# Kernel tuning notes

Hardware: AMD Instinct MI355X
Metric: run time of the kernel (lower is better)

## Reference

```python
import jax, jax.numpy as jnp
import numpy as np

D_MODEL = 256
N_LAYERS = 4
D_STATE = 16
D_CONV = 4
EXPAND = 2
HEADDIM = 64
D_INNER = EXPAND * D_MODEL            # 512
NHEADS = D_INNER // HEADDIM           # 8
CONV_DIM = D_INNER + 2 * D_STATE      # 544 (ngroups=1)
D_IN_PROJ = 2 * D_INNER + 2 * D_STATE + NHEADS  # 1064
VOCAB = 8
MAXLEN = 2048
NCLASSES = 2
PAD_IDX = 4
EPS = 1e-5
B, L = 8, 2048


def setup_inputs() -> dict:
    key = jax.random.key(0)
    ks = jax.random.split(key, 10)
    x = jax.random.randint(ks[0], (B, L), 0, VOCAB)
    attention_mask = jnp.ones((B, L), jnp.float32)
    embedding = 0.02 * jax.random.normal(ks[1], (VOCAB, D_MODEL), jnp.float32)
    embedding = embedding.at[PAD_IDX].set(0.0)  # padding_idx row is zero
    pos_embedding = 0.02 * jax.random.normal(ks[2], (1, MAXLEN, D_MODEL), jnp.float32)
    in_proj_w = 0.05 * jax.random.normal(ks[3], (N_LAYERS, D_IN_PROJ, D_MODEL), jnp.float32)
    conv_w = 0.3 * jax.random.normal(ks[4], (N_LAYERS, CONV_DIM, D_CONV), jnp.float32)
    conv_b = jnp.zeros((N_LAYERS, CONV_DIM), jnp.float32)
    # dt_bias = softplus^{-1}(dt) with dt ~ U(0.001, 0.1), as in mamba_ssm init
    dt = jax.random.uniform(ks[5], (N_LAYERS, NHEADS), jnp.float32, 0.001, 0.1)
    dt_bias = jnp.log(jnp.expm1(dt))
    A_log = jnp.log(jax.random.uniform(ks[6], (N_LAYERS, NHEADS), jnp.float32, 1.0, 16.0))
    D_param = jnp.ones((N_LAYERS, NHEADS), jnp.float32)
    norm_w = jnp.ones((N_LAYERS, D_INNER), jnp.float32)
    out_proj_w = 0.05 * jax.random.normal(ks[7], (N_LAYERS, D_MODEL, D_INNER), jnp.float32)
    ln_w = jnp.ones((D_MODEL,), jnp.float32)
    ln_b = jnp.zeros((D_MODEL,), jnp.float32)
    cls_w = 0.05 * jax.random.normal(ks[8], (NCLASSES, D_MODEL), jnp.float32)
    cls_b = jnp.zeros((NCLASSES,), jnp.float32)
    return dict(x=x, attention_mask=attention_mask, embedding=embedding,
                pos_embedding=pos_embedding, in_proj_w=in_proj_w, conv_w=conv_w,
                conv_b=conv_b, dt_bias=dt_bias, A_log=A_log, D_param=D_param,
                norm_w=norm_w, out_proj_w=out_proj_w, ln_w=ln_w, ln_b=ln_b,
                cls_w=cls_w, cls_b=cls_b)


def _mamba2(h_in, Wi, cw, cb, dtb, Alog, Dp, nw, Wo):
    """One Mamba2 block (ngroups=1, headdim=64, norm_before_gate=False)."""
    b, l, _ = h_in.shape
    zxbcdt = jnp.einsum('bld,ed->ble', h_in, Wi)          # (b,l,1064)
    z = zxbcdt[..., :D_INNER]                             # gate
    xBC = zxbcdt[..., D_INNER:D_INNER + CONV_DIM]
    dt = jax.nn.softplus(zxbcdt[..., D_INNER + CONV_DIM:] + dtb)  # (b,l,h)
    # causal depthwise conv1d (kernel D_CONV) + silu
    xp = jnp.pad(xBC, ((0, 0), (D_CONV - 1, 0), (0, 0)))
    xwin = jnp.stack([xp[:, k:k + l, :] for k in range(D_CONV)], axis=-1)  # (b,l,c,k)
    xBC = jax.nn.silu(jnp.einsum('blck,ck->blc', xwin, cw) + cb)
    xs = xBC[..., :D_INNER].reshape(b, l, NHEADS, HEADDIM)
    Bm = xBC[..., D_INNER:D_INNER + D_STATE]              # (b,l,n)
    Cm = xBC[..., D_INNER + D_STATE:]                     # (b,l,n)
    dA = jnp.exp(dt * (-jnp.exp(Alog)))                   # (b,l,h)
    dtx = dt[..., None] * xs                              # (b,l,h,p)

    def step(h, inp):
        dA_t, dtx_t, B_t, C_t = inp
        h = dA_t[:, :, None, None] * h + dtx_t[..., None] * B_t[:, None, None, :]
        y = jnp.einsum('bhpn,bn->bhp', h, C_t)
        return h, y

    h0 = jnp.zeros((b, NHEADS, HEADDIM, D_STATE), h_in.dtype)
    _, ys = jax.lax.scan(step, h0, (jnp.swapaxes(dA, 0, 1), jnp.swapaxes(dtx, 0, 1),
                                    jnp.swapaxes(Bm, 0, 1), jnp.swapaxes(Cm, 0, 1)))
    y = jnp.swapaxes(ys, 0, 1) + Dp[None, None, :, None] * xs  # skip term D*x
    y = y.reshape(b, l, D_INNER) * jax.nn.silu(z)               # gate, then RMSNorm
    y = y * jax.lax.rsqrt(jnp.mean(jnp.square(y), axis=-1, keepdims=True) + EPS) * nw
    return jnp.einsum('ble,de->bld', y, Wo)


def _layer_norm(h, w, b):
    mu = jnp.mean(h, -1, keepdims=True)
    var = jnp.mean(jnp.square(h - mu), -1, keepdims=True)
    return (h - mu) * jax.lax.rsqrt(var + EPS) * w + b


def reference(x, attention_mask, embedding, pos_embedding, in_proj_w, conv_w,
              conv_b, dt_bias, A_log, D_param, norm_w, out_proj_w, ln_w, ln_b,
              cls_w, cls_b):
    l = x.shape[1]
    h = embedding[x] + pos_embedding[:, :l, :]
    m = attention_mask[..., None]
    h = h * m
    for i in range(N_LAYERS):
        res = h
        h = _mamba2(h, in_proj_w[i], conv_w[i], conv_b[i], dt_bias[i],
                    A_log[i], D_param[i], norm_w[i], out_proj_w[i])
        h = _layer_norm(h + res, ln_w, ln_b)
        h = h * m
    pooled = jnp.mean(h, axis=1)   # dropout is identity at eval
    return pooled @ cls_w.T + cls_b
```

## Files before the change

kernel.cpp:

```cpp
#include <hip/hip_runtime.h>
#include <hip/hip_bf16.h>
#include <math.h>

#define B_ 8
#define L_ 2048
#define DM 256
#define DIP 1064
#define DI 512
#define CD 544
#define DSZ 16
#define NH 8
#define HD 64
#define Q_ 64
#define NC 32
#define ZST 76

typedef __attribute__((ext_vector_type(8))) short bf16x8;
typedef __attribute__((ext_vector_type(4))) float f32x4;

__device__ inline unsigned short f2bf(float f) {
    __hip_bfloat16 h = __float2bfloat16(f);
    return *(unsigned short*)&h;
}
__device__ inline float bf2f(unsigned short u) {
    unsigned int x = ((unsigned int)u) << 16;
    return __uint_as_float(x);
}
__device__ inline float fast_sig(float x) {
    return __builtin_amdgcn_rcpf(1.f + __expf(-x));
}

__global__ __launch_bounds__(256) void k_f2bf(const float* __restrict__ in, unsigned short* __restrict__ out, int n4) {
    int i = blockIdx.x * 256 + threadIdx.x;
    if (i >= n4) return;
    float4 v = *(const float4*)(in + (size_t)i * 4);
    ushort4 o;
    o.x = f2bf(v.x); o.y = f2bf(v.y); o.z = f2bf(v.z); o.w = f2bf(v.w);
    *(ushort4*)(out + (size_t)i * 4) = o;
}

__global__ __launch_bounds__(256) void k_embed(const int* __restrict__ x, const float* __restrict__ mask,
                                               const float* __restrict__ emb, const float* __restrict__ pos,
                                               unsigned short* __restrict__ h_bf) {
    int i = blockIdx.x * 256 + threadIdx.x;
    if (i >= B_ * L_ * DM) return;
    int d = i % DM;
    int bl = i / DM;
    int l = bl % L_;
    int tok = x[bl];
    float v = (emb[tok * DM + d] + pos[l * DM + d]) * mask[bl];
    h_bf[i] = f2bf(v);
}

__global__ __launch_bounds__(256) void k_gemm_in(const unsigned short* __restrict__ A,
                                                 const unsigned short* __restrict__ Bw,
                                                 unsigned short* __restrict__ Cb, float* __restrict__ dtraw) {
    const int lda = DM, ldb = DM, ldc = DIP, N = DIP, K = DM;
    __shared__ unsigned short Al[2][128 * 32];
    __shared__ unsigned short Bl[2][128 * 32];
    int tid = threadIdx.x;
    int l = tid & 63;
    int w = tid >> 6, wr = w >> 1, wc = w & 1;

    int wg = blockIdx.x;
    int xcd = wg & 7;
    int rest = wg >> 3;
    int mgrp = rest / 9;
    int n_tile = rest - mgrp * 9;
    int m_tile = xcd * 16 + mgrp;
    int m0 = m_tile * 128, n0 = n_tile * 128;

    f32x4 zero = {0.f, 0.f, 0.f, 0.f};
    f32x4 acc[4][4];
#pragma unroll
    for (int i = 0; i < 4; i++)
#pragma unroll
        for (int j = 0; j < 4; j++) acc[i][j] = zero;

    int lr = l & 15, kq = l >> 4;
    int aoff = (wr * 64 + lr) * 32 + kq * 8;
    int boff = (wc * 64 + lr) * 32 + kq * 8;

    auto stage = [&](int ks, int buf) {
        int k0 = ks * 32;
#pragma unroll
        for (int q = 0; q < 2; q++) {
            int c = tid + q * 256;
            int row = c >> 2, cc = (c & 3) * 8;
            const unsigned short* ga = A + (size_t)(m0 + row) * lda + k0 + cc;
            __builtin_amdgcn_global_load_lds((const __attribute__((address_space(1))) void*)ga,
                                             (__attribute__((address_space(3))) void*)(&Al[buf][c * 8]), 16, 0, 0);
            int rowb = n0 + row;
            if (rowb > N - 1) rowb = N - 1;
            const unsigned short* gb = Bw + (size_t)rowb * ldb + k0 + cc;
            __builtin_amdgcn_global_load_lds((const __attribute__((address_space(1))) void*)gb,
                                             (__attribute__((address_space(3))) void*)(&Bl[buf][c * 8]), 16, 0, 0);
        }
    };

    stage(0, 0);
    int ksteps = K / 32;
    for (int s = 0; s < ksteps; s++) {
        int buf = s & 1;
        __syncthreads();
        if (s + 1 < ksteps) stage(s + 1, buf ^ 1);
        bf16x8 a[4], b[4];
#pragma unroll
        for (int i = 0; i < 4; i++) a[i] = *(const bf16x8*)&Al[buf][aoff + i * 512];
#pragma unroll
        for (int j = 0; j < 4; j++) b[j] = *(const bf16x8*)&Bl[buf][boff + j * 512];
#pragma unroll
        for (int i = 0; i < 4; i++)
#pragma unroll
            for (int j = 0; j < 4; j++)
                acc[i][j] = __builtin_amdgcn_mfma_f32_16x16x32_bf16(a[i], b[j], acc[i][j], 0, 0, 0);
    }

#pragma unroll
    for (int i = 0; i < 4; i++) {
        int m = m0 + wr * 64 + i * 16 + kq * 4;
#pragma unroll
        for (int j = 0; j < 4; j++) {
            int n = n0 + wc * 64 + j * 16 + lr;
            if (n < N) {
#pragma unroll
                for (int r = 0; r < 4; r++)
                    Cb[(size_t)(m + r) * ldc + n] = f2bf(acc[i][j][r]);
                if (n >= DI + CD) {
#pragma unroll
                    for (int r = 0; r < 4; r++)
                        dtraw[(size_t)(m + r) * NH + (n - (DI + CD))] = acc[i][j][r];
                }
            }
        }
    }
}

__global__ __launch_bounds__(256) void k_gemm_ln(const unsigned short* __restrict__ A,
                                                 const unsigned short* __restrict__ Bw,
                                                 unsigned short* __restrict__ hbf,
                                                 const float* __restrict__ lnw, const float* __restrict__ lnb,
                                                 const float* __restrict__ mask) {
    __shared__ unsigned short Al[2][32 * 32];
    __shared__ unsigned short Bl[2][256 * 32];
    __shared__ float part_s[32][4], part_q[32][4];
    int tid = threadIdx.x;
    int l = tid & 63;
    int w = tid >> 6;
    int m0 = blockIdx.x * 32;
    int lr = l & 15, kq = l >> 4;

    f32x4 zero = {0.f, 0.f, 0.f, 0.f};
    f32x4 acc[2][4];
#pragma unroll
    for (int i = 0; i < 2; i++)
#pragma unroll
        for (int j = 0; j < 4; j++) acc[i][j] = zero;

    auto stage = [&](int ks, int buf) {
        int k0 = ks * 32;
        if (tid < 128) {
            int row = tid >> 2, cc = (tid & 3) * 8;
            const unsigned short* ga = A + (size_t)(m0 + row) * DI + k0 + cc;
            __builtin_amdgcn_global_load_lds((const __attribute__((address_space(1))) void*)ga,
                                             (__attribute__((address_space(3))) void*)(&Al[buf][tid * 8]), 16, 0, 0);
        }
#pragma unroll
        for (int q = 0; q < 4; q++) {
            int c = tid + q * 256;
            int row = c >> 2, cc = (c & 3) * 8;
            const unsigned short* gb = Bw + (size_t)row * DI + k0 + cc;
            __builtin_amdgcn_global_load_lds((const __attribute__((address_space(1))) void*)gb,
                                             (__attribute__((address_space(3))) void*)(&Bl[buf][c * 8]), 16, 0, 0);
        }
    };

    stage(0, 0);
    const int ksteps = DI / 32;
    for (int s = 0; s < ksteps; s++) {
        int buf = s & 1;
        __syncthreads();
        if (s + 1 < ksteps) stage(s + 1, buf ^ 1);
        bf16x8 a[2], b[4];
#pragma unroll
        for (int i = 0; i < 2; i++) a[i] = *(const bf16x8*)&Al[buf][(i * 16 + lr) * 32 + kq * 8];
#pragma unroll
        for (int j = 0; j < 4; j++) b[j] = *(const bf16x8*)&Bl[buf][(w * 64 + j * 16 + lr) * 32 + kq * 8];
#pragma unroll
        for (int i = 0; i < 2; i++)
#pragma unroll
            for (int j = 0; j < 4; j++)
                acc[i][j] = __builtin_amdgcn_mfma_f32_16x16x32_bf16(a[i], b[j], acc[i][j], 0, 0, 0);
    }

#pragma unroll
    for (int i = 0; i < 2; i++) {
#pragma unroll
        for (int r = 0; r < 4; r++) {
            int row = i * 16 + kq * 4 + r;
            const unsigned short* hrow = hbf + (size_t)(m0 + row) * DM + w * 64 + lr;
#pragma unroll
            for (int j = 0; j < 4; j++)
                acc[i][j][r] += bf2f(hrow[j * 16]);
        }
    }
#pragma unroll
    for (int i = 0; i < 2; i++) {
#pragma unroll
        for (int r = 0; r < 4; r++) {
            float sv = acc[i][0][r] + acc[i][1][r] + acc[i][2][r] + acc[i][3][r];
            float qv = acc[i][0][r] * acc[i][0][r] + acc[i][1][r] * acc[i][1][r] +
                       acc[i][2][r] * acc[i][2][r] + acc[i][3][r] * acc[i][3][r];
#pragma unroll
            for (int off = 1; off < 16; off <<= 1) {
                sv += __shfl_xor(sv, off);
                qv += __shfl_xor(qv, off);
            }
            if (lr == 0) {
                int row = i * 16 + kq * 4 + r;
                part_s[row][w] = sv;
                part_q[row][w] = qv;
            }
        }
    }
    __syncthreads();
    float4 wv4 = make_float4(lnw[w * 64 + 0 * 16 + lr], lnw[w * 64 + 1 * 16 + lr],
                             lnw[w * 64 + 2 * 16 + lr], lnw[w * 64 + 3 * 16 + lr]);
    float4 bv4 = make_float4(lnb[w * 64 + 0 * 16 + lr], lnb[w * 64 + 1 * 16 + lr],
                             lnb[w * 64 + 2 * 16 + lr], lnb[w * 64 + 3 * 16 + lr]);
#pragma unroll
    for (int i = 0; i < 2; i++) {
#pragma unroll
        for (int r = 0; r < 4; r++) {
            int row = i * 16 + kq * 4 + r;
            float sum = part_s[row][0] + part_s[row][1] + part_s[row][2] + part_s[row][3];
            float sq  = part_q[row][0] + part_q[row][1] + part_q[row][2] + part_q[row][3];
            float mu = sum * (1.f / DM);
            float var = sq * (1.f / DM) - mu * mu;
            float rs = rsqrtf(var + 1e-5f);
            float mk = mask[m0 + row];
            unsigned short* drow = hbf + (size_t)(m0 + row) * DM + w * 64 + lr;
            float wr_[4] = {wv4.x, wv4.y, wv4.z, wv4.w};
            float br_[4] = {bv4.x, bv4.y, bv4.z, bv4.w};
#pragma unroll
            for (int j = 0; j < 4; j++) {
                float o = ((acc[i][j][r] - mu) * rs * wr_[j] + br_[j]) * mk;
                drow[j * 16] = f2bf(o);
            }
        }
    }
}

__global__ __launch_bounds__(256) void k_bcdt(const unsigned short* __restrict__ zxb,
                                              const float* __restrict__ cw, const float* __restrict__ cb,
                                              const float* __restrict__ dtraw, const float* __restrict__ dtb,
                                              const float* __restrict__ Alog,
                                              unsigned short* __restrict__ BCc,
                                              float* __restrict__ dts_g, float* __restrict__ coefS_g,
                                              float* __restrict__ cumL, float* __restrict__ Pg) {
    int pair = blockIdx.x;
    int b = pair >> 5, c = pair & 31;
    int t0 = c * Q_;
    int tid = threadIdx.x;
    int t = tid & 63, oct = tid >> 6;
    {
        int lg0 = t0 + t - 3;
        const unsigned short* base = zxb + ((size_t)b * L_ + lg0) * DIP + 1024 + oct * 8;
        bf16x8 rows[4];
#pragma unroll
        for (int k = 0; k < 4; k++) {
            if (lg0 + k >= 0) rows[k] = *(const bf16x8*)(base + (size_t)k * DIP);
            else {
#pragma unroll
                for (int j = 0; j < 8; j++) rows[k][j] = 0;
            }
        }
        bf16x8 o;
#pragma unroll
        for (int j = 0; j < 8; j++) {
            int cc = DI + oct * 8 + j;
            float acc = cb[cc];
            acc = fmaf(bf2f((unsigned short)rows[0][j]), cw[cc * 4 + 0], acc);
            acc = fmaf(bf2f((unsigned short)rows[1][j]), cw[cc * 4 + 1], acc);
            acc = fmaf(bf2f((unsigned short)rows[2][j]), cw[cc * 4 + 2], acc);
            acc = fmaf(bf2f((unsigned short)rows[3][j]), cw[cc * 4 + 3], acc);
            float s = acc * fast_sig(acc);
            o[j] = (short)f2bf(s);
        }
        *(bf16x8*)(BCc + ((size_t)(b * L_ + t0 + t)) * 32 + oct * 8) = o;
    }
#pragma unroll
    for (int ho = 0; ho < 2; ho++) {
        int h = oct * 2 + ho;
        int bh = b * 8 + h;
        float raw = dtraw[(size_t)(b * L_ + t0 + t) * NH + h] + dtb[h];
        float dtv = (raw > 20.f) ? raw : log1pf(__expf(raw));
        float v = -__expf(Alog[h]) * dtv;
#pragma unroll
        for (int off = 1; off < 64; off <<= 1) {
            float u = __shfl_up(v, off);
            if (t >= off) v += u;
        }
        float lend = __shfl(v, 63);
        size_t base = (size_t)(bh * NC + c) * Q_ + t;
        dts_g[base] = dtv;
        cumL[base] = v;
        coefS_g[base] = __expf(lend - v) * dtv;
        if (t == 63) Pg[bh * NC + c] = __expf(v);
    }
}

__global__ __launch_bounds__(256) void k_scan1c(const unsigned short* __restrict__ zxb,
                                                const unsigned short* __restrict__ BCc,
                                                const float* __restrict__ dts_g, const float* __restrict__ coefS_g,
                                                const float* __restrict__ cumL,
                                                const float* __restrict__ cw, const float* __restrict__ cb,
                                                const float* __restrict__ Dp,
                                                unsigned short* __restrict__ ybuf, unsigned short* __restrict__ Sg) {
    int wg = blockIdx.x;
    int xcd = wg & 7;
    int rest = wg >> 3;
    int slot = rest >> 3;
    int h = rest & 7;
    int pair = slot * 8 + xcd;
    int b = pair >> 5, c = pair & 31;
    int bh = b * 8 + h;
    int tid = threadIdx.x;
    int t0 = c * Q_;
    int w = tid >> 6, l = tid & 63;
    int lr = l & 15, kq = l >> 4;

    __shared__ __align__(16) unsigned short Zl[67 * ZST];
    __shared__ __align__(16) unsigned short Xt[Q_ * 72];
    __shared__ __align__(16) unsigned short Cbf[Q_ * 32];
    __shared__ __align__(16) unsigned short Bbf[Q_ * 32];
    __shared__ __align__(16) unsigned short Btw[DSZ * 72];
    __shared__ float Lc[Q_], dts[Q_], coefS[Q_];
    unsigned short* Mbf = Zl;

    float Dval = Dp[h];

    for (int idx = tid; idx < 67 * 8; idx += 256) {
        int rr = idx >> 3, seg = idx & 7;
        int lg = t0 - 3 + rr;
        bf16x8 v;
        if (lg >= 0) {
            v = *(const bf16x8*)(zxb + (size_t)(b * L_ + lg) * DIP + DI + h * HD + seg * 8);
        } else {
#pragma unroll
            for (int j = 0; j < 8; j++) v[j] = 0;
        }
        *(ushort4*)&Zl[rr * ZST + seg * 8]     = *(ushort4*)&v;
        *(ushort4*)&Zl[rr * ZST + seg * 8 + 4] = *((ushort4*)&v + 1);
    }
    {
        bf16x8 z8;
#pragma unroll
        for (int j = 0; j < 8; j++) z8[j] = 0;
        *(bf16x8*)&Cbf[tid * 8] = z8;
        *(bf16x8*)&Bbf[tid * 8] = z8;
    }
    if (tid < 64) {
        size_t base = (size_t)(bh * NC + c) * Q_ + tid;
        dts[tid] = dts_g[base];
        Lc[tid] = cumL[base];
        coefS[tid] = coefS_g[base];
    }
    __syncthreads();

    float xreg[4][4];
#pragma unroll
    for (int pt = 0; pt < 4; pt++) {
#pragma unroll
        for (int r = 0; r < 4; r++) {
            int t = w * 16 + kq * 4 + r;
            int p = pt * 16 + lr;
            int cc = h * HD + p;
            float acc = cb[cc];
#pragma unroll
            for (int k = 0; k < 4; k++)
                acc = fmaf(bf2f(Zl[(t + k) * ZST + p]), cw[cc * 4 + k], acc);
            float s = acc * fast_sig(acc);
            xreg[pt][r] = s;
            Xt[p * 72 + t] = f2bf(s);
        }
    }
    {
        int t = tid & 63, oct = tid >> 6;
        bf16x8 v = *(const bf16x8*)(BCc + ((size_t)(b * L_ + t0 + t)) * 32 + oct * 8);
        float dtv = dts[t], cfv = coefS[t];
#pragma unroll
        for (int j = 0; j < 8; j++) {
            int n32 = oct * 8 + j;
            float s = bf2f((unsigned short)v[j]);
            if (n32 < 16) {
                int n = n32;
                Bbf[t * 32 + (((n >> 3) ^ (t & 3)) * 8) + (n & 7)] = f2bf(dtv * s);
                Btw[n * 72 + t] = f2bf(cfv * s);
            } else {
                int n = n32 - 16;
                Cbf[t * 32 + (((n >> 3) ^ (t & 3)) * 8) + (n & 7)] = (unsigned short)v[j];
            }
        }
    }
    __syncthreads();

    f32x4 zero = {0.f, 0.f, 0.f, 0.f};

    f32x4 cbt[4];
    {
        bf16x8 af = *(const bf16x8*)&Cbf[(w * 16 + lr) * 32 + ((kq ^ (lr & 3)) * 8)];
#pragma unroll
        for (int st = 0; st < 4; st++) {
            bf16x8 bf = *(const bf16x8*)&Bbf[(st * 16 + lr) * 32 + ((kq ^ (lr & 3)) * 8)];
            cbt[st] = __builtin_amdgcn_mfma_f32_16x16x32_bf16(af, bf, zero, 0, 0, 0);
        }
    }
#pragma unroll
    for (int st = 0; st < 4; st++) {
#pragma unroll
        for (int r = 0; r < 4; r++) {
            int t = w * 16 + kq * 4 + r;
            int s = st * 16 + lr;
            float m = (s <= t) ? __expf(Lc[t] - Lc[s]) * cbt[st][r] : 0.f;
            Mbf[t * 64 + (((s >> 3) ^ (t & 7)) * 8) + (s & 7)] = f2bf(m);
        }
    }
    __syncthreads();

    {
        unsigned short* base_y = ybuf + ((size_t)b * L_ + t0) * DI + h * HD;
        f32x4 acc[4];
#pragma unroll
        for (int pt = 0; pt < 4; pt++) acc[pt] = zero;
#pragma unroll
        for (int ks = 0; ks < 2; ks++) {
            bf16x8 af = *(const bf16x8*)&Mbf[(w * 16 + lr) * 64 + (((ks * 4 + kq) ^ (lr & 7)) * 8)];
#pragma unroll
            for (int pt = 0; pt < 4; pt++) {
                bf16x8 bf = *(const bf16x8*)&Xt[(pt * 16 + lr) * 72 + ks * 32 + kq * 8];
                acc[pt] = __builtin_amdgcn_mfma_f32_16x16x32_bf16(af, bf, acc[pt], 0, 0, 0);
            }
        }
#pragma unroll
        for (int pt = 0; pt < 4; pt++) {
#pragma unroll
            for (int r = 0; r < 4; r++) {
                int t = w * 16 + kq * 4 + r;
                int p = pt * 16 + lr;
                base_y[(size_t)t * DI + p] = f2bf(acc[pt][r] + Dval * xreg[pt][r]);
            }
        }
    }

    {
        f32x4 sacc = zero;
#pragma unroll
        for (int ks = 0; ks < 2; ks++) {
            bf16x8 af = *(const bf16x8*)&Xt[(w * 16 + lr) * 72 + ks * 32 + kq * 8];
            bf16x8 bf = *(const bf16x8*)&Btw[lr * 72 + ks * 32 + kq * 8];
            sacc = __builtin_amdgcn_mfma_f32_16x16x32_bf16(af, bf, sacc, 0, 0, 0);
        }
#pragma unroll
        for (int r = 0; r < 4; r++) {
            int p = w * 16 + kq * 4 + r;
            Sg[((size_t)(bh * NC + c) * HD + p) * DSZ + lr] = f2bf(sacc[r]);
        }
    }
}

__global__ __launch_bounds__(256) void k_scan2(const unsigned short* __restrict__ Sg, const float* __restrict__ Pg,
                                               unsigned short* __restrict__ Hg) {
    int bh = blockIdx.x;
    int tid = threadIdx.x;
    int p = tid >> 2, n0 = (tid & 3) * 4;
    float4 H = make_float4(0.f, 0.f, 0.f, 0.f);
    for (int g = 0; g < NC / 8; g++) {
        ushort4 S[8];
#pragma unroll
        for (int j = 0; j < 8; j++)
            S[j] = *(const ushort4*)(Sg + (((size_t)bh * NC + g * 8 + j) * HD + p) * DSZ + n0);
#pragma unroll
        for (int j = 0; j < 8; j++) {
            int cc = g * 8 + j;
            ushort4 ho;
            ho.x = f2bf(H.x); ho.y = f2bf(H.y); ho.z = f2bf(H.z); ho.w = f2bf(H.w);
            *(ushort4*)(Hg + (((size_t)bh * NC + cc) * HD + p) * DSZ + n0) = ho;
            float P = Pg[bh * NC + cc];
            H.x = fmaf(P, H.x, bf2f(S[j].x));
            H.y = fmaf(P, H.y, bf2f(S[j].y));
            H.z = fmaf(P, H.z, bf2f(S[j].z));
            H.w = fmaf(P, H.w, bf2f(S[j].w));
        }
    }
}

__global__ __launch_bounds__(256) void k_scan3g(const unsigned short* __restrict__ ybuf,
                                                const unsigned short* __restrict__ zxb,
                                                const unsigned short* __restrict__ Hg, const float* __restrict__ cumLg,
                                                const unsigned short* __restrict__ BCc, const float* __restrict__ nw,
                                                unsigned short* __restrict__ yn_bf) {
    int b = blockIdx.x, by = blockIdx.y;
    int c64 = by >> 2, tl0 = (by & 3) * 16;
    int t0 = by * 16;
    int tid = threadIdx.x;
    __shared__ float Hsn[DSZ * 576];
    __shared__ float Lq[NH][16];

    {
        int p = tid & 63, hp = tid >> 6;
#pragma unroll
        for (int ho = 0; ho < 2; ho++) {
            int hh = hp * 2 + ho;
            const unsigned short* src = Hg + (((size_t)(b * NH + hh) * NC + c64) * HD + p) * DSZ;
            float* dst = &Hsn[p * 9 + hh];
            bf16x8 lo = *(const bf16x8*)(src);
            bf16x8 hi = *(const bf16x8*)(src + 8);
#pragma unroll
            for (int nq = 0; nq < 8; nq++) {
                dst[nq * 576] = bf2f((unsigned short)lo[nq]);
                dst[(nq + 8) * 576] = bf2f((unsigned short)hi[nq]);
            }
        }
    }
    if (tid < 128) {
        int hh = tid >> 4, t = tid & 15;
        Lq[hh][t] = cumLg[((size_t)(b * NH + hh) * NC + c64) * Q_ + tl0 + t];
    }
    __syncthreads();

    int t = tid >> 4, q = tid & 15;
    int hh = q >> 1, p0 = (q & 1) * 32;
    size_t bl = (size_t)b * L_ + t0 + t;
    float ef = __expf(Lq[hh][t]);

    float Cr[16];
    {
        const unsigned short* crow = BCc + bl * 32 + 16;
        bf16x8 lo = *(const bf16x8*)(crow);
        bf16x8 hi = *(const bf16x8*)(crow + 8);
#pragma unroll
        for (int k = 0; k < 8; k++) {
            Cr[k] = ef * bf2f((unsigned short)lo[k]);
            Cr[k + 8] = ef * bf2f((unsigned short)hi[k]);
        }
    }

    const unsigned short* yrow = ybuf + bl * DI + hh * HD + p0;
    const unsigned short* zrow = zxb + bl * DIP + hh * HD + p0;
    unsigned short yv[32], zv[32];
#pragma unroll
    for (int k = 0; k < 4; k++) *(bf16x8*)&yv[k * 8] = *(const bf16x8*)(yrow + k * 8);
#pragma unroll
    for (int k = 0; k < 4; k++) *(bf16x8*)&zv[k * 8] = *(const bf16x8*)(zrow + k * 8);

    float yg[32];
    float ss = 0.f;
#pragma unroll
    for (int j = 0; j < 32; j++) {
        const float* hp_ = &Hsn[(p0 + j) * 9 + hh];
        float d = 0.f;
#pragma unroll
        for (int n = 0; n < DSZ; n++) d = fmaf(Cr[n], hp_[n * 576], d);
        float y = bf2f(yv[j]) + d;
        float z = bf2f(zv[j]);
        yg[j] = y * z * fast_sig(z);
        ss = fmaf(yg[j], yg[j], ss);
    }
    ss += __shfl_xor(ss, 1);
    ss += __shfl_xor(ss, 2);
    ss += __shfl_xor(ss, 4);
    ss += __shfl_xor(ss, 8);
    float r = rsqrtf(ss * (1.f / DI) + 1e-5f);

    const float* nwp = nw + hh * HD + p0;
    unsigned short* dst = yn_bf + bl * DI + hh * HD + p0;
#pragma unroll
    for (int k = 0; k < 4; k++) {
        bf16x8 o;
#pragma unroll
        for (int j = 0; j < 8; j++) o[j] = (short)f2bf(yg[k * 8 + j] * r * nwp[k * 8 + j]);
        *(bf16x8*)(dst + k * 8) = o;
    }
}

__global__ __launch_bounds__(256) void k_pool1(const unsigned short* __restrict__ h, float* __restrict__ part) {
    int b = blockIdx.x, g = blockIdx.y, d = threadIdx.x;
    const unsigned short* hb = h + ((size_t)b * L_ + g * 128) * DM + d;
    float s = 0.f;
    for (int l = 0; l < 128; l++) s += bf2f(hb[(size_t)l * DM]);
    part[((size_t)b * 16 + g) * DM + d] = s;
}

__global__ __launch_bounds__(256) void k_pool2(const float* __restrict__ part, const float* __restrict__ cw,
                                               const float* __restrict__ cb, float* __restrict__ out) {
    int b = blockIdx.x, tid = threadIdx.x;
    float s = 0.f;
#pragma unroll
    for (int g = 0; g < 16; g++) s += part[((size_t)b * 16 + g) * DM + tid];
    s *= (1.0f / L_);
    float p0 = s * cw[tid];
    float p1 = s * cw[DM + tid];
#pragma unroll
    for (int m = 1; m < 64; m <<= 1) {
        p0 += __shfl_xor(p0, m);
        p1 += __shfl_xor(p1, m);
    }
    __shared__ float r0[4], r1[4];
    if ((tid & 63) == 0) { r0[tid >> 6] = p0; r1[tid >> 6] = p1; }
    __syncthreads();
    if (tid == 0) {
        out[b * 2 + 0] = r0[0] + r0[1] + r0[2] + r0[3] + cb[0];
        out[b * 2 + 1] = r1[0] + r1[1] + r1[2] + r1[3] + cb[1];
    }
}

extern "C" void kernel_launch(void* const* d_in, const int* in_sizes, int n_in,
                              void* d_out, int out_size, void* d_ws, size_t ws_size,
                              hipStream_t stream) {
    const int*   x    = (const int*)d_in[0];
    const float* mask = (const float*)d_in[1];
    const float* emb  = (const float*)d_in[2];
    const float* pos  = (const float*)d_in[3];
    const float* Wi   = (const float*)d_in[4];
    const float* cw   = (const float*)d_in[5];
    const float* cb   = (const float*)d_in[6];
    const float* dtb  = (const float*)d_in[7];
    const float* Alog = (const float*)d_in[8];
    const float* Dp   = (const float*)d_in[9];
    const float* nw   = (const float*)d_in[10];
    const float* Wo   = (const float*)d_in[11];
    const float* lnw  = (const float*)d_in[12];
    const float* lnb  = (const float*)d_in[13];
    const float* clsw = (const float*)d_in[14];
    const float* clsb = (const float*)d_in[15];
    float* out = (float*)d_out;

    float* ws     = (float*)d_ws;
    float* dtraw  = ws;
    float* Pg     = dtraw + (size_t)B_ * L_ * NH;
    float* cumL   = Pg + (size_t)64 * NC;
    float* dts_g  = cumL + (size_t)64 * NC * Q_;
    float* coefSg = dts_g + (size_t)64 * NC * Q_;
    float* pool   = coefSg + (size_t)64 * NC * Q_;
    unsigned short* Sg    = (unsigned short*)(pool + (size_t)B_ * 16 * DM);
    unsigned short* Hg    = Sg + (size_t)64 * NC * HD * DSZ;
    unsigned short* BCc   = Hg + (size_t)64 * NC * HD * DSZ;
    unsigned short* zxb   = BCc + (size_t)B_ * L_ * 32;
    unsigned short* ybuf  = zxb + (size_t)B_ * L_ * DIP;
    unsigned short* h_bf  = ybuf + (size_t)B_ * L_ * DI;
    unsigned short* yn_bf = h_bf + (size_t)B_ * L_ * DM;
    unsigned short* Wi_bf = yn_bf + (size_t)B_ * L_ * DI;
    unsigned short* Wo_bf = Wi_bf + (size_t)4 * DIP * DM;

    k_f2bf<<<(4 * DIP * DM / 4 + 255) / 256, 256, 0, stream>>>(Wi, Wi_bf, 4 * DIP * DM / 4);
    k_f2bf<<<(4 * DM * DI / 4 + 255) / 256, 256, 0, stream>>>(Wo, Wo_bf, 4 * DM * DI / 4);

    k_embed<<<(B_ * L_ * DM + 255) / 256, 256, 0, stream>>>(x, mask, emb, pos, h_bf);

    for (int i = 0; i < 4; i++) {
        k_gemm_in<<<128 * 9, 256, 0, stream>>>(
            h_bf, Wi_bf + (size_t)i * DIP * DM, zxb, dtraw);
        k_bcdt<<<B_ * NC, 256, 0, stream>>>(
            zxb, cw + (size_t)i * CD * 4, cb + i * CD, dtraw, dtb + i * NH, Alog + i * NH,
            BCc, dts_g, coefSg, cumL, Pg);
        k_scan1c<<<2048, 256, 0, stream>>>(
            zxb, BCc, dts_g, coefSg, cumL, cw + (size_t)i * CD * 4, cb + i * CD,
            Dp + i * NH, ybuf, Sg);
        k_scan2<<<64, 256, 0, stream>>>(Sg, Pg, Hg);
        k_scan3g<<<dim3(B_, 128), 256, 0, stream>>>(ybuf, zxb, Hg, cumL, BCc, nw + (size_t)i * DI, yn_bf);
        k_gemm_ln<<<B_ * L_ / 32, 256, 0, stream>>>(
            yn_bf, Wo_bf + (size_t)i * DM * DI, h_bf, lnw, lnb, mask);
    }

    k_pool1<<<dim3(B_, 16), 256, 0, stream>>>(h_bf, pool);
    k_pool2<<<B_, 256, 0, stream>>>(pool, clsw, clsb, out);
}
```

Before: 363.3 us.

## Enlarge out-proj GEMM tile to 64 rows and stage scan y output through LDS

The out-projection GEMM with fused LayerNorm now runs 512 threads per block over 64 rows instead of 32, as a 2x4 wave grid. Each weight tile loaded into LDS is therefore reused across twice as many rows, which halves the weight traffic per output row. The scan kernel now writes its y tile into a shared buffer (aliased over the C/B buffers) and then stores it to global memory as coalesced 16-byte vectors instead of scattered 2-byte stores. This adds a barrier and uses more LDS per block, which can lower occupancy, and there are half as many GEMM blocks.

```diff
diff --git a/kernel.cpp b/kernel.cpp
--- a/kernel.cpp
+++ b/kernel.cpp
@@ -136,18 +136,19 @@
     }
 }
 
-__global__ __launch_bounds__(256) void k_gemm_ln(const unsigned short* __restrict__ A,
+__global__ __launch_bounds__(512) void k_gemm_ln(const unsigned short* __restrict__ A,
                                                  const unsigned short* __restrict__ Bw,
                                                  unsigned short* __restrict__ hbf,
                                                  const float* __restrict__ lnw, const float* __restrict__ lnb,
                                                  const float* __restrict__ mask) {
-    __shared__ unsigned short Al[2][32 * 32];
+    __shared__ unsigned short Al[2][64 * 32];
     __shared__ unsigned short Bl[2][256 * 32];
-    __shared__ float part_s[32][4], part_q[32][4];
+    __shared__ float part_s[64][4], part_q[64][4];
     int tid = threadIdx.x;
     int l = tid & 63;
-    int w = tid >> 6;
-    int m0 = blockIdx.x * 32;
+    int w8 = tid >> 6;
+    int wr = w8 >> 2, wc = w8 & 3;
+    int m0 = blockIdx.x * 64;
     int lr = l & 15, kq = l >> 4;
 
     f32x4 zero = {0.f, 0.f, 0.f, 0.f};
@@ -159,15 +160,15 @@
 
     auto stage = [&](int ks, int buf) {
         int k0 = ks * 32;
-        if (tid < 128) {
+        if (tid < 256) {
             int row = tid >> 2, cc = (tid & 3) * 8;
             const unsigned short* ga = A + (size_t)(m0 + row) * DI + k0 + cc;
             __builtin_amdgcn_global_load_lds((const __attribute__((address_space(1))) void*)ga,
                                              (__attribute__((address_space(3))) void*)(&Al[buf][tid * 8]), 16, 0, 0);
         }
 #pragma unroll
-        for (int q = 0; q < 4; q++) {
-            int c = tid + q * 256;
+        for (int q = 0; q < 2; q++) {
+            int c = tid + q * 512;
             int row = c >> 2, cc = (c & 3) * 8;
             const unsigned short* gb = Bw + (size_t)row * DI + k0 + cc;
             __builtin_amdgcn_global_load_lds((const __attribute__((address_space(1))) void*)gb,
@@ -183,9 +184,9 @@
         if (s + 1 < ksteps) stage(s + 1, buf ^ 1);
         bf16x8 a[2], b[4];
 #pragma unroll
-        for (int i = 0; i < 2; i++) a[i] = *(const bf16x8*)&Al[buf][(i * 16 + lr) * 32 + kq * 8];
-#pragma unroll
-        for (int j = 0; j < 4; j++) b[j] = *(const bf16x8*)&Bl[buf][(w * 64 + j * 16 + lr) * 32 + kq * 8];
+        for (int i = 0; i < 2; i++) a[i] = *(const bf16x8*)&Al[buf][(wr * 32 + i * 16 + lr) * 32 + kq * 8];
+#pragma unroll
+        for (int j = 0; j < 4; j++) b[j] = *(const bf16x8*)&Bl[buf][(wc * 64 + j * 16 + lr) * 32 + kq * 8];
 #pragma unroll
         for (int i = 0; i < 2; i++)
 #pragma unroll
@@ -197,8 +198,8 @@
     for (int i = 0; i < 2; i++) {
 #pragma unroll
         for (int r = 0; r < 4; r++) {
-            int row = i * 16 + kq * 4 + r;
-            const unsigned short* hrow = hbf + (size_t)(m0 + row) * DM + w * 64 + lr;
+            int row = wr * 32 + i * 16 + kq * 4 + r;
+            const unsigned short* hrow = hbf + (size_t)(m0 + row) * DM + wc * 64 + lr;
 #pragma unroll
             for (int j = 0; j < 4; j++)
                 acc[i][j][r] += bf2f(hrow[j * 16]);
@@ -217,29 +218,29 @@
                 qv += __shfl_xor(qv, off);
             }
             if (lr == 0) {
-                int row = i * 16 + kq * 4 + r;
-                part_s[row][w] = sv;
-                part_q[row][w] = qv;
+                int row = wr * 32 + i * 16 + kq * 4 + r;
+                part_s[row][wc] = sv;
+                part_q[row][wc] = qv;
             }
         }
     }
     __syncthreads();
-    float4 wv4 = make_float4(lnw[w * 64 + 0 * 16 + lr], lnw[w * 64 + 1 * 16 + lr],
-                             lnw[w * 64 + 2 * 16 + lr], lnw[w * 64 + 3 * 16 + lr]);
-    float4 bv4 = make_float4(lnb[w * 64 + 0 * 16 + lr], lnb[w * 64 + 1 * 16 + lr],
-                             lnb[w * 64 + 2 * 16 + lr], lnb[w * 64 + 3 * 16 + lr]);
+    float4 wv4 = make_float4(lnw[wc * 64 + 0 * 16 + lr], lnw[wc * 64 + 1 * 16 + lr],
+                             lnw[wc * 64 + 2 * 16 + lr], lnw[wc * 64 + 3 * 16 + lr]);
+    float4 bv4 = make_float4(lnb[wc * 64 + 0 * 16 + lr], lnb[wc * 64 + 1 * 16 + lr],
+                             lnb[wc * 64 + 2 * 16 + lr], lnb[wc * 64 + 3 * 16 + lr]);
 #pragma unroll
     for (int i = 0; i < 2; i++) {
 #pragma unroll
         for (int r = 0; r < 4; r++) {
-            int row = i * 16 + kq * 4 + r;
+            int row = wr * 32 + i * 16 + kq * 4 + r;
             float sum = part_s[row][0] + part_s[row][1] + part_s[row][2] + part_s[row][3];
             float sq  = part_q[row][0] + part_q[row][1] + part_q[row][2] + part_q[row][3];
             float mu = sum * (1.f / DM);
             float var = sq * (1.f / DM) - mu * mu;
             float rs = rsqrtf(var + 1e-5f);
             float mk = mask[m0 + row];
-            unsigned short* drow = hbf + (size_t)(m0 + row) * DM + w * 64 + lr;
+            unsigned short* drow = hbf + (size_t)(m0 + row) * DM + wc * 64 + lr;
             float wr_[4] = {wv4.x, wv4.y, wv4.z, wv4.w};
             float br_[4] = {bv4.x, bv4.y, bv4.z, bv4.w};
 #pragma unroll
@@ -332,11 +333,13 @@
 
     __shared__ __align__(16) unsigned short Zl[67 * ZST];
     __shared__ __align__(16) unsigned short Xt[Q_ * 72];
-    __shared__ __align__(16) unsigned short Cbf[Q_ * 32];
-    __shared__ __align__(16) unsigned short Bbf[Q_ * 32];
+    __shared__ __align__(16) unsigned short Pool[4096];
     __shared__ __align__(16) unsigned short Btw[DSZ * 72];
     __shared__ float Lc[Q_], dts[Q_], coefS[Q_];
     unsigned short* Mbf = Zl;
+    unsigned short* Cbf = Pool;
+    unsigned short* Bbf = Pool + 2048;
+    unsigned short* Ylds = Pool;
 
     float Dval = Dp[h];
 
@@ -429,7 +432,6 @@
     __syncthreads();
 
     {
-        unsigned short* base_y = ybuf + ((size_t)b * L_ + t0) * DI + h * HD;
         f32x4 acc[4];
 #pragma unroll
         for (int pt = 0; pt < 4; pt++) acc[pt] = zero;
@@ -448,7 +450,7 @@
             for (int r = 0; r < 4; r++) {
                 int t = w * 16 + kq * 4 + r;
                 int p = pt * 16 + lr;
-                base_y[(size_t)t * DI + p] = f2bf(acc[pt][r] + Dval * xreg[pt][r]);
+                Ylds[t * 64 + p] = f2bf(acc[pt][r] + Dval * xreg[pt][r]);
             }
         }
     }
@@ -465,6 +467,17 @@
         for (int r = 0; r < 4; r++) {
             int p = w * 16 + kq * 4 + r;
             Sg[((size_t)(bh * NC + c) * HD + p) * DSZ + lr] = f2bf(sacc[r]);
+        }
+    }
+    __syncthreads();
+
+    {
+        unsigned short* base_y = ybuf + ((size_t)b * L_ + t0) * DI + h * HD;
+#pragma unroll
+        for (int q = 0; q < 2; q++) {
+            int idx = q * 256 + tid;
+            int t = idx >> 3, oct = idx & 7;
+            *(bf16x8*)(base_y + (size_t)t * DI + oct * 8) = *(const bf16x8*)&Ylds[t * 64 + oct * 8];
         }
     }
 }
@@ -669,7 +682,7 @@
             Dp + i * NH, ybuf, Sg);
         k_scan2<<<64, 256, 0, stream>>>(Sg, Pg, Hg);
         k_scan3g<<<dim3(B_, 128), 256, 0, stream>>>(ybuf, zxb, Hg, cumL, BCc, nw + (size_t)i * DI, yn_bf);
-        k_gemm_ln<<<B_ * L_ / 32, 256, 0, stream>>>(
+        k_gemm_ln<<<B_ * L_ / 64, 512, 0, stream>>>(
             yn_bf, Wo_bf + (size_t)i * DM * DI, h_bf, lnw, lnb, mask);
     }
 
```

Measured after the change: 366.0 us. No clear change (+0.7%).
